# Performance work log

Hardware: AMD Instinct MI355X
Metric: run time of the kernel (lower is better)

The kernel has to match this reference:

```python
import jax, jax.numpy as jnp
import numpy as np

B, T = 64, 512
VOCAB, E, H = 20, 64, 128
D = 2 * H            # 256, bidirectional LSTM output dim
NH, KD = 8, D // 8   # 8 heads, key_dim 32
DU, OUT = 256, 128
NEG = -1e9


def _lstm_scan(x, mask, W, U, b):
    # x: [B,T,E], mask: [B,T] bool. Keras gate order: i, f, g(c), o.
    Bb = x.shape[0]
    Hh = U.shape[0]
    def step(carry, inp):
        h, c = carry
        xt, mt = inp                      # [B,E], [B]
        z = xt @ W + h @ U + b            # [B,4H]
        i, f, g, o = jnp.split(z, 4, axis=-1)
        c_new = jax.nn.sigmoid(f) * c + jax.nn.sigmoid(i) * jnp.tanh(g)
        h_new = jax.nn.sigmoid(o) * jnp.tanh(c_new)
        m = mt[:, None]
        h = jnp.where(m, h_new, h)        # freeze state/output on masked steps
        c = jnp.where(m, c_new, c)
        return (h, c), h
    h0 = jnp.zeros((Bb, Hh), x.dtype)
    _, ys = jax.lax.scan(step, (h0, h0), (jnp.swapaxes(x, 0, 1), mask.T))
    return jnp.swapaxes(ys, 0, 1)         # [B,T,H]


def setup_inputs() -> dict:
    key = jax.random.key(0)
    ks = jax.random.split(key, 24)
    g = lambda k, shape, s: (jax.random.normal(k, shape, jnp.float32) * s)
    inp = {
        'sequences': jax.random.randint(ks[0], (B, T), 0, VOCAB),
        'emb': g(ks[1], (VOCAB, E), 0.05),
        # forward LSTM
        'Wf': g(ks[2], (E, 4 * H), 0.05), 'Uf': g(ks[3], (H, 4 * H), 0.05), 'bf': jnp.zeros((4 * H,), jnp.float32),
        # backward LSTM
        'Wb': g(ks[4], (E, 4 * H), 0.05), 'Ub': g(ks[5], (H, 4 * H), 0.05), 'bb': jnp.zeros((4 * H,), jnp.float32),
        # MHA projections
        'Wq': g(ks[6], (D, NH, KD), 0.05), 'bq': jnp.zeros((NH, KD), jnp.float32),
        'Wk': g(ks[7], (D, NH, KD), 0.05), 'bk': jnp.zeros((NH, KD), jnp.float32),
        'Wv': g(ks[8], (D, NH, KD), 0.05), 'bv': jnp.zeros((NH, KD), jnp.float32),
        'Wo': g(ks[9], (NH, KD, D), 0.05), 'bo': jnp.zeros((D,), jnp.float32),
        # MLP head (input is concat of avg+max pool -> 2*D)
        'W1': g(ks[10], (2 * D, DU), 0.05), 'b1': jnp.zeros((DU,), jnp.float32),
        'W2': g(ks[11], (DU, DU // 2), 0.05), 'b2': jnp.zeros((DU // 2,), jnp.float32),
        'W3': g(ks[12], (DU // 2, OUT), 0.05), 'b3': jnp.zeros((OUT,), jnp.float32),
    }
    return inp


def _forward(sequences, emb, Wf, Uf, bf, Wb, Ub, bb, Wq, bq, Wk, bk, Wv, bv, Wo, bo, W1, b1, W2, b2, W3, b3):
    mask = sequences != 0                       # mask_zero=True
    x = emb[sequences]                          # [B,T,E]
    fwd = _lstm_scan(x, mask, Wf, Uf, bf)
    bwd = _lstm_scan(x[:, ::-1], mask[:, ::-1], Wb, Ub, bb)[:, ::-1]
    h = jnp.concatenate([fwd, bwd], axis=-1)    # [B,T,D]
    # Multi-head self-attention (key-masked, Keras MHA math)
    q = jnp.einsum('btd,dhk->bthk', h, Wq) + bq
    k = jnp.einsum('btd,dhk->bthk', h, Wk) + bk
    v = jnp.einsum('btd,dhk->bthk', h, Wv) + bv
    scores = jnp.einsum('bthk,bshk->bhts', q, k) / jnp.sqrt(jnp.float32(KD))
    scores = jnp.where(mask[:, None, None, :], scores, NEG)
    attn = jax.nn.softmax(scores, axis=-1)      # [B,H,T,T]
    ctx = jnp.einsum('bhts,bshk->bthk', attn, v)
    att = jnp.einsum('bthk,hkd->btd', ctx, Wo) + bo   # [B,T,D]
    # dual pooling (masked mean + masked max)
    mf = mask[..., None].astype(att.dtype)
    avg = (att * mf).sum(axis=1) / jnp.maximum(mf.sum(axis=1), 1.0)
    mx = jnp.where(mask[..., None], att, NEG).max(axis=1)
    p = jnp.concatenate([avg, mx], axis=-1)     # [B,2D]
    x1 = jax.nn.relu(p @ W1 + b1)
    x2 = jax.nn.relu(x1 @ W2 + b2)
    return x2 @ W3 + b3                         # [B,OUT]


def reference(sequences, emb, Wf, Uf, bf, Wb, Ub, bb, Wq, bq, Wk, bk, Wv, bv, Wo, bo, W1, b1, W2, b2, W3, b3):
    return _forward(sequences, emb, Wf, Uf, bf, Wb, Ub, bb, Wq, bq, Wk, bk, Wv, bv, Wo, bo, W1, b1, W2, b2, W3, b3)
```

## Files before the change

### kernel.cpp

```cpp
#include <hip/hip_runtime.h>
#include <math.h>

#define B_ 64
#define T_ 512
#define E_ 64
#define H_ 128
#define NH_ 8
#define KD_ 32
#define BT_ (B_ * T_)
#define NEG_ -1e9f

typedef __attribute__((ext_vector_type(8))) short bf16x8_t;
typedef __attribute__((ext_vector_type(4))) float f32x4_t;
typedef __attribute__((ext_vector_type(2))) float f32x2_t;
typedef unsigned short ushort_t;
typedef unsigned int uint_t;

__device__ __forceinline__ float sigmoidf_(float x) {
    return 1.f / (1.f + __expf(-x));
}
__device__ __forceinline__ float tanhf_(float x) {
    return 1.f - 2.f / (1.f + __expf(2.f * x));
}

__device__ __forceinline__ ushort_t bf16_rne(float x) {
    uint_t u = __float_as_uint(x);
    uint_t r = (u + 0x7FFFu + ((u >> 16) & 1u)) >> 16;
    return (ushort_t)r;
}
__device__ __forceinline__ float bf16_to_f(ushort_t h) {
    return __uint_as_float(((uint_t)h) << 16);
}
__device__ __forceinline__ void split_bf16(float x, ushort_t& h, ushort_t& l) {
    h = bf16_rne(x);
    l = bf16_rne(x - bf16_to_f(h));
}

__device__ __forceinline__ float qswap1(float x) {
    return __int_as_float(__builtin_amdgcn_mov_dpp(__float_as_int(x), 0xB1, 0xF, 0xF, true));
}

__global__ void prep_kernel(
    const float* __restrict__ emb,
    const float* __restrict__ Wf, const float* __restrict__ bf,
    const float* __restrict__ Wb, const float* __restrict__ bb,
    const float* __restrict__ Wq, const float* __restrict__ Wk,
    const float* __restrict__ Wv, const float* __restrict__ Wo,
    const float* __restrict__ bq, const float* __restrict__ bk,
    const float* __restrict__ bv,
    ushort_t* __restrict__ wqkvh, ushort_t* __restrict__ wqkvl,
    ushort_t* __restrict__ woh, ushort_t* __restrict__ wol,
    float* __restrict__ embWf, float* __restrict__ embWb,
    float* __restrict__ qkvb)
{
    const int blk = blockIdx.x, tid = threadIdx.x;
    if (blk < 1024) {
        const int m = blk >> 8, k = blk & 255;
        const float* W = (m == 0) ? Wq : (m == 1) ? Wk : (m == 2) ? Wv : Wo;
        float v = W[k * 256 + tid];
        ushort_t h, l;
        split_bf16(v, h, l);
        if (m < 3) {
            wqkvh[(m * 256 + tid) * 256 + k] = h;
            wqkvl[(m * 256 + tid) * 256 + k] = l;
        } else {
            woh[tid * 256 + k] = h;
            wol[tid * 256 + k] = l;
        }
    } else if (blk < 1028) {
        const int e = blk - 1024;
        const int dir = e >> 1, half = e & 1;
        const float* W = dir ? Wb : Wf;
        const float* bias = dir ? bb : bf;
        float* dst = dir ? embWb : embWf;
        const int np = half * 256 + tid;
        const int gin = ((np & 3) << 7) + (np >> 2);
        for (int v = 0; v < 20; ++v) {
            float acc = bias[gin];
            for (int k = 0; k < 64; ++k)
                acc = fmaf(emb[v * 64 + k], W[k * 512 + gin], acc);
            dst[v * 512 + np] = acc;
        }
    } else {
        qkvb[tid] = bq[tid];
        qkvb[256 + tid] = bk[tid];
        qkvb[512 + tid] = bv[tid];
    }
}

__global__ __launch_bounds__(256, 2) void gemm_mfma3(
    const ushort_t* __restrict__ Ah, const ushort_t* __restrict__ Al,
    const ushort_t* __restrict__ Bh, const ushort_t* __restrict__ Bl,
    const float* __restrict__ bias, float* __restrict__ C,
    int M, int N)
{
    __shared__ __align__(16) ushort_t Alds[2][128 * 40];
    __shared__ __align__(16) ushort_t Blds[2][128 * 40];

    const int tid = threadIdx.x;
    const int ntn = N >> 7;
    const int bm = blockIdx.x / ntn, bn = blockIdx.x % ntn;
    const int m0 = bm << 7, n0 = bn << 7;

    const int w = tid >> 6;
    const int wr = w >> 1, wc = w & 1;
    const int lane = tid & 63;
    const int fr = lane & 15, kg = lane >> 4;

    const int sr = tid >> 1;
    const int sh = (tid & 1) << 4;

    f32x4_t acc[4][4];
#pragma unroll
    for (int i = 0; i < 4; ++i)
#pragma unroll
        for (int j = 0; j < 4; ++j) acc[i][j] = (f32x4_t){0.f, 0.f, 0.f, 0.f};

    for (int ks = 0; ks < 8; ++ks) {
        const int k0 = ks << 5;
        __syncthreads();
        {
            const size_t ga = (size_t)(m0 + sr) * 256 + k0 + sh;
            const size_t gb = (size_t)(n0 + sr) * 256 + k0 + sh;
            const int ld = sr * 40 + sh;
            const uint4* pah = (const uint4*)(Ah + ga);
            const uint4* pal = (const uint4*)(Al + ga);
            const uint4* pbh = (const uint4*)(Bh + gb);
            const uint4* pbl = (const uint4*)(Bl + gb);
            uint4* qah = (uint4*)&Alds[0][ld];
            uint4* qal = (uint4*)&Alds[1][ld];
            uint4* qbh = (uint4*)&Blds[0][ld];
            uint4* qbl = (uint4*)&Blds[1][ld];
            qah[0] = pah[0]; qah[1] = pah[1];
            qal[0] = pal[0]; qal[1] = pal[1];
            qbh[0] = pbh[0]; qbh[1] = pbh[1];
            qbl[0] = pbl[0]; qbl[1] = pbl[1];
        }
        __syncthreads();

        bf16x8_t ah[4], al[4], bh[4], bl[4];
#pragma unroll
        for (int i = 0; i < 4; ++i) {
            const int ra = (wr * 64 + i * 16 + fr) * 40 + kg * 8;
            const int rb = (wc * 64 + i * 16 + fr) * 40 + kg * 8;
            ah[i] = *(const bf16x8_t*)&Alds[0][ra];
            al[i] = *(const bf16x8_t*)&Alds[1][ra];
            bh[i] = *(const bf16x8_t*)&Blds[0][rb];
            bl[i] = *(const bf16x8_t*)&Blds[1][rb];
        }
#pragma unroll
        for (int i = 0; i < 4; ++i)
#pragma unroll
            for (int j = 0; j < 4; ++j) {
                acc[i][j] = __builtin_amdgcn_mfma_f32_16x16x32_bf16(
                    ah[i], bh[j], acc[i][j], 0, 0, 0);
                acc[i][j] = __builtin_amdgcn_mfma_f32_16x16x32_bf16(
                    ah[i], bl[j], acc[i][j], 0, 0, 0);
                acc[i][j] = __builtin_amdgcn_mfma_f32_16x16x32_bf16(
                    al[i], bh[j], acc[i][j], 0, 0, 0);
            }
    }

#pragma unroll
    for (int j = 0; j < 4; ++j) {
        const int col = n0 + wc * 64 + j * 16 + fr;
        const float bv = bias[col];
#pragma unroll
        for (int i = 0; i < 4; ++i) {
#pragma unroll
            for (int r = 0; r < 4; ++r) {
                const int row = m0 + wr * 64 + i * 16 + kg * 4 + r;
                C[(size_t)row * N + col] = acc[i][j][r] + bv;
            }
        }
    }
}

__global__ __launch_bounds__(256, 1) void lstm_scan(
    const int* __restrict__ seq,
    const float* __restrict__ embWf, const float* __restrict__ embWb,
    const float* __restrict__ Uf, const float* __restrict__ Ub,
    ushort_t* __restrict__ hch, ushort_t* __restrict__ hcl)
{
    const int w = blockIdx.x;
    const int dir = w & 1, b = w >> 1;
    const float* eW = dir ? embWb : embWf;
    const float* U  = dir ? Ub  : Uf;
    const int tid = threadIdx.x;
    const int jj = tid >> 1, ks = tid & 1;

    __shared__ __align__(16) float eWl[20 * 512];
    __shared__ __align__(16) float hbuf[2][136];
    __shared__ int tkl[T_];

    f32x2_t u2[4][32];
#pragma unroll
    for (int g = 0; g < 4; ++g)
#pragma unroll
        for (int c = 0; c < 32; ++c) {
            const int kb_ = 64 * ks + 2 * c;
            u2[g][c] = (f32x2_t){
                U[(size_t)kb_ * 512 + g * 128 + jj],
                U[(size_t)(kb_ + 1) * 512 + g * 128 + jj] };
        }

    {
        const float4* src = (const float4*)eW;
        float4* dst = (float4*)eWl;
        for (int i = tid; i < 2560; i += 256) dst[i] = src[i];
        tkl[tid] = seq[b * T_ + tid];
        tkl[tid + 256] = seq[b * T_ + 256 + tid];
        for (int i = tid; i < 272; i += 256) ((float*)hbuf)[i] = 0.f;
    }

    float h_cur = 0.f, c_cur = 0.f;
    ushort_t* hoh = hch + (size_t)b * T_ * 256 + dir * 128;
    ushort_t* hol = hcl + (size_t)b * T_ * 256 + dir * 128;

    __syncthreads();

    int te = dir ? (T_ - 1) : 0;
    int tok = tkl[te];
    float4 xwv = *(const float4*)&eWl[tok * 512 + jj * 4];

    int p = 0;
    for (int t = 0; t < T_; ++t) {
        const int te_n  = dir ? (te - 1) : (te + 1);
        const int te_pf = (t == T_ - 1) ? te : te_n;
        const int tok_n = tkl[te_pf];
        const float4 xw_n = *(const float4*)&eWl[tok_n * 512 + jj * 4];

        f32x2_t ac0 = {0.f, 0.f}, ac1 = {0.f, 0.f};
        f32x2_t ac2 = {0.f, 0.f}, ac3 = {0.f, 0.f};
        const f32x2_t* hc2 = (const f32x2_t*)&hbuf[p][68 * ks];
#pragma unroll
        for (int c = 0; c < 32; ++c) {
            const f32x2_t h2 = hc2[c];
            ac0 = __builtin_elementwise_fma(h2, u2[0][c], ac0);
            ac1 = __builtin_elementwise_fma(h2, u2[1][c], ac1);
            ac2 = __builtin_elementwise_fma(h2, u2[2][c], ac2);
            ac3 = __builtin_elementwise_fma(h2, u2[3][c], ac3);
        }
        float a0 = ac0.x + ac0.y, a1 = ac1.x + ac1.y;
        float a2 = ac2.x + ac2.y, a3 = ac3.x + ac3.y;
        a0 += qswap1(a0);
        a1 += qswap1(a1);
        a2 += qswap1(a2);
        a3 += qswap1(a3);

        const float zi = xwv.x + a0, zf = xwv.y + a1;
        const float zg = xwv.z + a2, zo = xwv.w + a3;
        const float cn = fmaf(sigmoidf_(zf), c_cur, sigmoidf_(zi) * tanhf_(zg));
        const float hn = sigmoidf_(zo) * tanhf_(cn);
        const bool mt = (tok != 0);
        const float hm = mt ? hn : h_cur;
        c_cur = mt ? cn : c_cur;
        h_cur = hm;

        if (ks == 0) {
            const int pos = (jj < 64) ? jj : jj + 4;
            hbuf[1 - p][pos] = hm;
            ushort_t hh, hl;
            split_bf16(hm, hh, hl);
            hoh[(size_t)te * 256 + jj] = hh;
            hol[(size_t)te * 256 + jj] = hl;
        }
        asm volatile("s_waitcnt lgkmcnt(0)\n\ts_barrier" ::: "memory");
        p ^= 1; te = te_n; tok = tok_n; xwv = xw_n;
    }
}

__global__ __launch_bounds__(256, 2) void attn_fused(
    const int* __restrict__ seq,
    const float* __restrict__ qkv,
    ushort_t* __restrict__ cxh, ushort_t* __restrict__ cxl)
{
    const int wg = blockIdx.x;
    const int b = wg >> 3, h = wg & 7;
    const int tid = threadIdx.x;

    __shared__ __align__(16) float Ks[16][32];
    __shared__ __align__(16) float Vs[16][32];
    __shared__ float mk[16];

    float qA[32], qB[32];
    {
        const float* qp  = qkv + ((size_t)(b * T_) + tid) * 768 + h * KD_;
        const float* qp2 = qp + (size_t)256 * 768;
#pragma unroll
        for (int k = 0; k < 32; k += 4) {
            float4 v0 = *(const float4*)(qp + k);
            float4 v1 = *(const float4*)(qp2 + k);
            qA[k] = v0.x; qA[k + 1] = v0.y; qA[k + 2] = v0.z; qA[k + 3] = v0.w;
            qB[k] = v1.x; qB[k + 1] = v1.y; qB[k + 2] = v1.z; qB[k + 3] = v1.w;
        }
    }
    float ctxA[32], ctxB[32];
#pragma unroll
    for (int k = 0; k < 32; ++k) { ctxA[k] = 0.f; ctxB[k] = 0.f; }
    float mA = -1e30f, mB = -1e30f, lA = 0.f, lB = 0.f;

    const int lr = (tid & 127) >> 3;
    const int lc = (tid & 7) << 2;
    const bool loadV = (tid >= 128);

    for (int c = 0; c < T_ / 16; ++c) {
        const int s0 = c << 4;
        __syncthreads();
        {
            const float* src = qkv + ((size_t)(b * T_) + s0 + lr) * 768 +
                               (loadV ? 512 : 256) + h * KD_ + lc;
            float4 v = *(const float4*)src;
            if (loadV) *(float4*)&Vs[lr][lc] = v;
            else       *(float4*)&Ks[lr][lc] = v;
            if (tid < 16) mk[tid] = (seq[b * T_ + s0 + tid] != 0) ? 0.f : 1.f;
        }
        __syncthreads();

        float sA[16], sB[16];
#pragma unroll
        for (int s = 0; s < 16; ++s) {
            float dA = 0.f, dB = 0.f;
#pragma unroll
            for (int k = 0; k < 32; k += 4) {
                float4 k4 = *(const float4*)&Ks[s][k];
                dA = fmaf(k4.x, qA[k], dA); dA = fmaf(k4.y, qA[k + 1], dA);
                dA = fmaf(k4.z, qA[k + 2], dA); dA = fmaf(k4.w, qA[k + 3], dA);
                dB = fmaf(k4.x, qB[k], dB); dB = fmaf(k4.y, qB[k + 1], dB);
                dB = fmaf(k4.z, qB[k + 2], dB); dB = fmaf(k4.w, qB[k + 3], dB);
            }
            const float SCL = 0.17677669529663687f;
            const bool masked = (mk[s] > 0.5f);
            sA[s] = masked ? NEG_ : dA * SCL;
            sB[s] = masked ? NEG_ : dB * SCL;
        }
        float cmA = sA[0], cmB = sB[0];
#pragma unroll
        for (int s = 1; s < 16; ++s) {
            cmA = fmaxf(cmA, sA[s]); cmB = fmaxf(cmB, sB[s]);
        }
        const float mnA = fmaxf(mA, cmA), mnB = fmaxf(mB, cmB);
        const float alA = __expf(mA - mnA), alB = __expf(mB - mnB);
        float psA = 0.f, psB = 0.f;
#pragma unroll
        for (int s = 0; s < 16; ++s) {
            float pa = __expf(sA[s] - mnA); sA[s] = pa; psA += pa;
            float pb = __expf(sB[s] - mnB); sB[s] = pb; psB += pb;
        }
        lA = fmaf(lA, alA, psA); lB = fmaf(lB, alB, psB);
        mA = mnA; mB = mnB;
#pragma unroll
        for (int k = 0; k < 32; ++k) { ctxA[k] *= alA; ctxB[k] *= alB; }
#pragma unroll
        for (int s = 0; s < 16; ++s) {
#pragma unroll
            for (int k = 0; k < 32; k += 4) {
                float4 v4 = *(const float4*)&Vs[s][k];
                ctxA[k]     = fmaf(sA[s], v4.x, ctxA[k]);
                ctxA[k + 1] = fmaf(sA[s], v4.y, ctxA[k + 1]);
                ctxA[k + 2] = fmaf(sA[s], v4.z, ctxA[k + 2]);
                ctxA[k + 3] = fmaf(sA[s], v4.w, ctxA[k + 3]);
                ctxB[k]     = fmaf(sB[s], v4.x, ctxB[k]);
                ctxB[k + 1] = fmaf(sB[s], v4.y, ctxB[k + 1]);
                ctxB[k + 2] = fmaf(sB[s], v4.z, ctxB[k + 2]);
                ctxB[k + 3] = fmaf(sB[s], v4.w, ctxB[k + 3]);
            }
        }
    }

    const float iA = 1.f / lA, iB = 1.f / lB;
    ushort_t* chA = cxh + (((size_t)(b * T_) + tid) * NH_ + h) * KD_;
    ushort_t* clA = cxl + (((size_t)(b * T_) + tid) * NH_ + h) * KD_;
    ushort_t* chB = chA + (size_t)256 * NH_ * KD_;
    ushort_t* clB = clA + (size_t)256 * NH_ * KD_;
#pragma unroll
    for (int k = 0; k < 32; ++k) {
        ushort_t hA, lA_, hB, lB_;
        split_bf16(ctxA[k] * iA, hA, lA_);
        split_bf16(ctxB[k] * iB, hB, lB_);
        chA[k] = hA; clA[k] = lA_;
        chB[k] = hB; clB[k] = lB_;
    }
}

__global__ __launch_bounds__(256) void poolmlp_kernel(
    const int* __restrict__ seq, const float* __restrict__ att,
    const float* __restrict__ W1, const float* __restrict__ b1,
    const float* __restrict__ W2, const float* __restrict__ b2,
    const float* __restrict__ W3, const float* __restrict__ b3,
    float* __restrict__ out)
{
    const int b = blockIdx.x;
    const int tid = threadIdx.x;
    __shared__ float mk[T_];
    __shared__ float pl[512];
    __shared__ float x1l[256];
    __shared__ float x2l[128];

    for (int t = tid; t < T_; t += 256)
        mk[t] = (seq[b * T_ + t] != 0) ? 1.f : 0.f;
    __syncthreads();

    float sum = 0.f, mx = NEG_, cnt = 0.f;
    for (int t = 0; t < T_; ++t) {
        const float a = att[((size_t)b * T_ + t) * 256 + tid];
        const float m = mk[t];
        cnt += m;
        sum = fmaf(m, a, sum);
        mx = fmaxf(mx, (m > 0.5f) ? a : NEG_);
    }
    pl[tid] = sum / fmaxf(cnt, 1.f);
    pl[256 + tid] = mx;
    __syncthreads();

    {
        float acc = b1[tid];
        for (int k = 0; k < 512; ++k) acc = fmaf(pl[k], W1[k * 256 + tid], acc);
        x1l[tid] = fmaxf(acc, 0.f);
    }
    __syncthreads();
    if (tid < 128) {
        float acc = b2[tid];
        for (int k = 0; k < 256; ++k) acc = fmaf(x1l[k], W2[k * 128 + tid], acc);
        x2l[tid] = fmaxf(acc, 0.f);
    }
    __syncthreads();
    if (tid < 128) {
        float acc = b3[tid];
        for (int k = 0; k < 128; ++k) acc = fmaf(x2l[k], W3[k * 128 + tid], acc);
        out[b * 128 + tid] = acc;
    }
}

extern "C" void kernel_launch(void* const* d_in, const int* in_sizes, int n_in,
                              void* d_out, int out_size, void* d_ws, size_t ws_size,
                              hipStream_t stream)
{
    (void)in_sizes; (void)n_in; (void)out_size; (void)ws_size;
    const int*   seq = (const int*)d_in[0];
    const float* emb = (const float*)d_in[1];
    const float* Wf  = (const float*)d_in[2];
    const float* Uf  = (const float*)d_in[3];
    const float* bf  = (const float*)d_in[4];
    const float* Wb  = (const float*)d_in[5];
    const float* Ub  = (const float*)d_in[6];
    const float* bb  = (const float*)d_in[7];
    const float* Wq  = (const float*)d_in[8];
    const float* bq  = (const float*)d_in[9];
    const float* Wk  = (const float*)d_in[10];
    const float* bk  = (const float*)d_in[11];
    const float* Wv  = (const float*)d_in[12];
    const float* bv  = (const float*)d_in[13];
    const float* Wo  = (const float*)d_in[14];
    const float* bo  = (const float*)d_in[15];
    const float* W1  = (const float*)d_in[16];
    const float* b1  = (const float*)d_in[17];
    const float* W2  = (const float*)d_in[18];
    const float* b2  = (const float*)d_in[19];
    const float* W3  = (const float*)d_in[20];
    const float* b3  = (const float*)d_in[21];
    float* out = (float*)d_out;
    float* ws  = (float*)d_ws;

    float* qkv  = ws;
    ushort_t* cxh = (ushort_t*)(ws + 25165824);
    ushort_t* cxl = cxh + (size_t)BT_ * 256;
    ushort_t* hch = (ushort_t*)(ws + 33554432);
    ushort_t* hcl = hch + (size_t)BT_ * 256;
    float* attb = ws + 33554432;
    ushort_t* wt = (ushort_t*)(ws + 41943040);
    ushort_t* wqkvh = wt;
    ushort_t* wqkvl = wt + 196608;
    ushort_t* woh   = wt + 393216;
    ushort_t* wol   = wt + 458752;
    float* embWf = ws + 41943040 + 262144;
    float* embWb = embWf + 20 * 512;
    float* qkvb  = embWb + 20 * 512;

    const dim3 blk256(256);

    prep_kernel<<<dim3(1029), blk256, 0, stream>>>(
        emb, Wf, bf, Wb, bb, Wq, Wk, Wv, Wo, bq, bk, bv,
        wqkvh, wqkvl, woh, wol, embWf, embWb, qkvb);

    lstm_scan<<<dim3(128), blk256, 0, stream>>>(
        seq, embWf, embWb, Uf, Ub, hch, hcl);

    gemm_mfma3<<<dim3((BT_ / 128) * 6), blk256, 0, stream>>>(
        hch, hcl, wqkvh, wqkvl, qkvb, qkv, BT_, 768);

    attn_fused<<<dim3(B_ * NH_), blk256, 0, stream>>>(seq, qkv, cxh, cxl);

    gemm_mfma3<<<dim3((BT_ / 128) * 2), blk256, 0, stream>>>(
        cxh, cxl, woh, wol, bo, attb, BT_, 256);

    poolmlp_kernel<<<dim3(B_), blk256, 0, stream>>>(
        seq, attb, W1, b1, W2, b2, W3, b3, out);
}
```

Baseline: 1.057 ms.

## Split LSTM recurrence across 8 lanes per hidden unit with 1024-thread blocks

The LSTM scan block grows from 256 to 1024 threads, so each hidden unit's recurrent dot product is split over 8 lanes instead of 2. Each lane now holds a quarter as many U values in registers, and the partial sums are combined with DPP and ds_swizzle reductions. The embedding-times-W table is no longer staged in LDS and is read from global memory each step. This shortens the serial per-step FMA chain but adds a longer cross-lane reduction and a per-step barrier across 16 waves instead of 4.

```diff
diff --git a/kernel.cpp b/kernel.cpp
--- a/kernel.cpp
+++ b/kernel.cpp
@@ -38,6 +38,12 @@
 
 __device__ __forceinline__ float qswap1(float x) {
     return __int_as_float(__builtin_amdgcn_mov_dpp(__float_as_int(x), 0xB1, 0xF, 0xF, true));
+}
+__device__ __forceinline__ float qswap2(float x) {
+    return __int_as_float(__builtin_amdgcn_mov_dpp(__float_as_int(x), 0x4E, 0xF, 0xF, true));
+}
+__device__ __forceinline__ float swz4(float x) {
+    return __int_as_float(__builtin_amdgcn_ds_swizzle(__float_as_int(x), 0x101F));
 }
 
 __global__ void prep_kernel(
@@ -176,7 +182,7 @@
     }
 }
 
-__global__ __launch_bounds__(256, 1) void lstm_scan(
+__global__ __launch_bounds__(1024, 4) void lstm_scan(
     const int* __restrict__ seq,
     const float* __restrict__ embWf, const float* __restrict__ embWb,
     const float* __restrict__ Uf, const float* __restrict__ Ub,
@@ -187,31 +193,24 @@
     const float* eW = dir ? embWb : embWf;
     const float* U  = dir ? Ub  : Uf;
     const int tid = threadIdx.x;
-    const int jj = tid >> 1, ks = tid & 1;
-
-    __shared__ __align__(16) float eWl[20 * 512];
-    __shared__ __align__(16) float hbuf[2][136];
+    const int jj = tid >> 3, ks = tid & 7;
+
+    __shared__ __align__(16) float hbuf[2][8][20];
     __shared__ int tkl[T_];
 
-    f32x2_t u2[4][32];
+    f32x2_t u2[4][8];
 #pragma unroll
     for (int g = 0; g < 4; ++g)
 #pragma unroll
-        for (int c = 0; c < 32; ++c) {
-            const int kb_ = 64 * ks + 2 * c;
+        for (int c = 0; c < 8; ++c) {
+            const int kb_ = 16 * ks + 2 * c;
             u2[g][c] = (f32x2_t){
                 U[(size_t)kb_ * 512 + g * 128 + jj],
                 U[(size_t)(kb_ + 1) * 512 + g * 128 + jj] };
         }
 
-    {
-        const float4* src = (const float4*)eW;
-        float4* dst = (float4*)eWl;
-        for (int i = tid; i < 2560; i += 256) dst[i] = src[i];
-        tkl[tid] = seq[b * T_ + tid];
-        tkl[tid + 256] = seq[b * T_ + 256 + tid];
-        for (int i = tid; i < 272; i += 256) ((float*)hbuf)[i] = 0.f;
-    }
+    if (tid < T_) tkl[tid] = seq[b * T_ + tid];
+    if (tid < 2 * 8 * 20) ((float*)hbuf)[tid] = 0.f;
 
     float h_cur = 0.f, c_cur = 0.f;
     ushort_t* hoh = hch + (size_t)b * T_ * 256 + dir * 128;
@@ -221,20 +220,20 @@
 
     int te = dir ? (T_ - 1) : 0;
     int tok = tkl[te];
-    float4 xwv = *(const float4*)&eWl[tok * 512 + jj * 4];
+    float4 xwv = *(const float4*)&eW[tok * 512 + jj * 4];
 
     int p = 0;
     for (int t = 0; t < T_; ++t) {
         const int te_n  = dir ? (te - 1) : (te + 1);
         const int te_pf = (t == T_ - 1) ? te : te_n;
         const int tok_n = tkl[te_pf];
-        const float4 xw_n = *(const float4*)&eWl[tok_n * 512 + jj * 4];
+        const float4 xw_n = *(const float4*)&eW[tok_n * 512 + jj * 4];
 
         f32x2_t ac0 = {0.f, 0.f}, ac1 = {0.f, 0.f};
         f32x2_t ac2 = {0.f, 0.f}, ac3 = {0.f, 0.f};
-        const f32x2_t* hc2 = (const f32x2_t*)&hbuf[p][68 * ks];
-#pragma unroll
-        for (int c = 0; c < 32; ++c) {
+        const f32x2_t* hc2 = (const f32x2_t*)&hbuf[p][ks][0];
+#pragma unroll
+        for (int c = 0; c < 8; ++c) {
             const f32x2_t h2 = hc2[c];
             ac0 = __builtin_elementwise_fma(h2, u2[0][c], ac0);
             ac1 = __builtin_elementwise_fma(h2, u2[1][c], ac1);
@@ -243,10 +242,12 @@
         }
         float a0 = ac0.x + ac0.y, a1 = ac1.x + ac1.y;
         float a2 = ac2.x + ac2.y, a3 = ac3.x + ac3.y;
-        a0 += qswap1(a0);
-        a1 += qswap1(a1);
-        a2 += qswap1(a2);
-        a3 += qswap1(a3);
+        a0 += qswap1(a0); a1 += qswap1(a1);
+        a2 += qswap1(a2); a3 += qswap1(a3);
+        a0 += qswap2(a0); a1 += qswap2(a1);
+        a2 += qswap2(a2); a3 += qswap2(a3);
+        a0 += swz4(a0); a1 += swz4(a1);
+        a2 += swz4(a2); a3 += swz4(a3);
 
         const float zi = xwv.x + a0, zf = xwv.y + a1;
         const float zg = xwv.z + a2, zo = xwv.w + a3;
@@ -258,8 +259,7 @@
         h_cur = hm;
 
         if (ks == 0) {
-            const int pos = (jj < 64) ? jj : jj + 4;
-            hbuf[1 - p][pos] = hm;
+            hbuf[1 - p][jj >> 4][jj & 15] = hm;
             ushort_t hh, hl;
             split_bf16(hm, hh, hl);
             hoh[(size_t)te * 256 + jj] = hh;
@@ -483,7 +483,7 @@
         emb, Wf, bf, Wb, bb, Wq, Wk, Wv, Wo, bq, bk, bv,
         wqkvh, wqkvl, woh, wol, embWf, embWb, qkvb);
 
-    lstm_scan<<<dim3(128), blk256, 0, stream>>>(
+    lstm_scan<<<dim3(128), dim3(1024), 0, stream>>>(
         seq, embWf, embWb, Uf, Ub, hch, hcl);
 
     gemm_mfma3<<<dim3((BT_ / 128) * 6), blk256, 0, stream>>>(
```

Result: slower. 1.170 ms (+10.7%).
